# Kernel optimization log

Hardware: AMD Instinct MI355X
Metric: run time of the kernel (lower is better)

## Reference

```python
import jax, jax.numpy as jnp
import numpy as np

IN_FEATURES = 3072
OUT_FEATURES = 4096
PADDED = 4096  # 2**ceil(log2(in_features))
PADDING = PADDED - IN_FEATURES
MIN_RANGE = -384.0
MAX_RANGE = 384.0
Q_LEVELS = 255.0  # 8-bit affine quantization


def fwht(x):
    """Unnormalized fast Walsh-Hadamard transform along the last axis.
    H @ H = n * I, matching the /padded_dim rescale in forward."""
    n = x.shape[-1]
    m = int(round(np.log2(n)))
    lead = x.shape[:-1]
    x = x.reshape((-1,) + (2,) * m)
    for ax in range(1, m + 1):  # m <= 12 fixed butterfly stages
        a = jnp.take(x, 0, axis=ax)
        b = jnp.take(x, 1, axis=ax)
        x = jnp.stack([a + b, a - b], axis=ax)
    return x.reshape(lead + (n,))


def quant_dequant(x):
    """QuantizedMatrix: clip to [MIN_RANGE, MAX_RANGE], 8-bit affine
    quantize, then dequantize (reference computes the dequantized values)."""
    scale = (MAX_RANGE - MIN_RANGE) / Q_LEVELS
    q = jnp.clip(jnp.round((jnp.clip(x, MIN_RANGE, MAX_RANGE) - MIN_RANGE) / scale), 0.0, Q_LEVELS)
    return q * scale + MIN_RANGE


def setup_inputs() -> dict:
    key = jax.random.key(0)
    k1, k2, k3 = jax.random.split(key, 3)
    x = jax.random.normal(k1, (2, 4096, IN_FEATURES), dtype=jnp.float32)
    weight = jax.random.normal(k2, (OUT_FEATURES, IN_FEATURES), dtype=jnp.float32)
    bias = jax.random.normal(k3, (OUT_FEATURES,), dtype=jnp.float32)
    return {"x": x, "weight": weight, "bias": bias}


def reference(x, weight, bias):
    # pad feature dim to power of two, Hadamard-rotate activations and weights
    xh = fwht(jnp.pad(x, ((0, 0), (0, 0), (0, PADDING))))          # [B,S,P]
    wh = fwht(jnp.pad(weight, ((0, 0), (0, PADDING))))              # [O,P]
    qx = quant_dequant(xh)
    qw = quant_dequant(wh)
    # qx @ qw / padded_dim + bias  (qw contracted over the padded dim)
    return jnp.einsum('bsp,op->bso', qx, qw) / PADDED + bias
```

## Files before the change

### kernel.cpp

```cpp
#include <hip/hip_runtime.h>

typedef int v4i __attribute__((ext_vector_type(4)));
typedef int v16i __attribute__((ext_vector_type(16)));

#define IN_F   3072
#define PAD    4096
#define M_ROWS 8192
#define N_OUT  4096

#define BM 128
#define BN 256
#define BK 64

__device__ __forceinline__ void async_copy16(const void* g, void* l) {
    __builtin_amdgcn_global_load_lds(
        (__attribute__((address_space(1))) const void*)(uintptr_t)g,
        (__attribute__((address_space(3))) void*)(uint32_t)(uintptr_t)l,
        16, 0, 0);
}

__device__ __forceinline__ void fwht16(float v[16]) {
#pragma unroll
    for (int s = 1; s < 16; s <<= 1) {
#pragma unroll
        for (int i = 0; i < 16; i++) {
            if ((i & s) == 0) {
                float a = v[i], b = v[i ^ s];
                v[i]     = a + b;
                v[i ^ s] = a - b;
            }
        }
    }
}

__global__ __launch_bounds__(256) void fwht_quant_kernel(
    const float* __restrict__ in, signed char* __restrict__ qout,
    int* __restrict__ rowsum, int nrows)
{
    __shared__ float lds[4096];
    __shared__ int ssum;
    const int t = threadIdx.x;
    const int r = blockIdx.x;
    if (r >= nrows) return;
    const float* row = in + (size_t)r * IN_F;

    float v[16];
#pragma unroll
    for (int j = 0; j < 16; j++)
        v[j] = (j < 12) ? row[j * 256 + t] : 0.0f;

    fwht16(v);

    const int th = t >> 4, tl = t & 15;

    #pragma unroll
    for (int j = 0; j < 16; j++)
        lds[256 * j + 16 * (th ^ j) + (tl ^ th)] = v[j];
    __syncthreads();
#pragma unroll
    for (int j = 0; j < 16; j++)
        v[j] = lds[256 * th + 16 * (j ^ th) + (tl ^ j)];

    fwht16(v);

    if (t == 0) ssum = 0;
    __syncthreads();

#pragma unroll
    for (int j = 0; j < 16; j++)
        lds[256 * th + 16 * (j ^ th) + (tl ^ j)] = v[j];
    __syncthreads();
#pragma unroll
    for (int j = 0; j < 16; j++)
        v[j] = lds[256 * th + 16 * (tl ^ th) + (j ^ tl)];

    fwht16(v);

    const float INV = 0.33203125f;
    int sum = 0;
    int pk[4];
#pragma unroll
    for (int c = 0; c < 4; c++) {
        int word = 0;
#pragma unroll
        for (int b = 0; b < 4; b++) {
            float x = v[c * 4 + b];
            x = fminf(fmaxf(x, -384.0f), 384.0f);
            float qf = rintf((x + 384.0f) * INV);
            int qi = (int)qf;
            qi = qi < 0 ? 0 : (qi > 255 ? 255 : qi);
            int a = qi - 128;
            sum += a;
            word |= (a & 255) << (8 * b);
        }
        pk[c] = word;
    }

#pragma unroll
    for (int off = 32; off > 0; off >>= 1) sum += __shfl_down(sum, off, 64);
    if ((t & 63) == 0) atomicAdd(&ssum, sum);

    ((int4*)(qout + (size_t)r * PAD))[t] = make_int4(pk[0], pk[1], pk[2], pk[3]);

    __syncthreads();
    if (t == 0) rowsum[r] = ssum;
}

__global__ __launch_bounds__(256, 2) void gemm_i8_kernel(
    const signed char* __restrict__ A, const signed char* __restrict__ B,
    const int* __restrict__ SA, const int* __restrict__ SB,
    const float* __restrict__ bias, float* __restrict__ out,
    float kA, float kS, float kC)
{
    __shared__ __align__(16) signed char As[BM * BK];
    __shared__ __align__(16) signed char Bs[BN * BK];

    const int tid  = threadIdx.x;
    const int lane = tid & 63;
    const int wid  = tid >> 6;
    const int wr   = wid >> 1, wc = wid & 1;
    const int bm   = blockIdx.y * BM;
    const int bn   = blockIdx.x * BN;
    const int l5   = lane >> 5;
    const int lm   = lane & 31;

    v16i acc[2][4];
#pragma unroll
    for (int i = 0; i < 2; i++)
#pragma unroll
        for (int j = 0; j < 4; j++)
#pragma unroll
            for (int e = 0; e < 16; e++)
                acc[i][j][e] = 0;

    for (int bk = 0; bk < PAD; bk += BK) {
#pragma unroll
        for (int i = 0; i < 2; i++) {
            int c = wid * 128 + i * 64 + lane;
            int rr = c >> 2, p = c & 3;
            int q = (p - rr) & 3;
            async_copy16(A + (size_t)(bm + rr) * PAD + bk + q * 16,
                         As + (wid * 128 + i * 64) * 16);
        }
#pragma unroll
        for (int i = 0; i < 4; i++) {
            int c = wid * 256 + i * 64 + lane;
            int rr = c >> 2, p = c & 3;
            int q = (p - rr) & 3;
            async_copy16(B + (size_t)(bn + rr) * PAD + bk + q * 16,
                         Bs + (wid * 256 + i * 64) * 16);
        }
        __syncthreads();

#pragma unroll
        for (int ks = 0; ks < 2; ks++) {
            const int qbase = ks * 2 + l5;
            v4i a[2], b[4];
#pragma unroll
            for (int mt = 0; mt < 2; mt++) {
                int rr = wr * 64 + mt * 32 + lm;
                int p = (qbase + rr) & 3;
                a[mt] = *(const v4i*)(As + rr * 64 + p * 16);
            }
#pragma unroll
            for (int nt = 0; nt < 4; nt++) {
                int rr = wc * 128 + nt * 32 + lm;
                int p = (qbase + rr) & 3;
                b[nt] = *(const v4i*)(Bs + rr * 64 + p * 16);
            }
#pragma unroll
            for (int mt = 0; mt < 2; mt++)
#pragma unroll
                for (int nt = 0; nt < 4; nt++)
                    acc[mt][nt] = __builtin_amdgcn_mfma_i32_32x32x32_i8(
                        a[mt], b[nt], acc[mt][nt], 0, 0, 0);
        }
        __syncthreads();
    }

#pragma unroll
    for (int nt = 0; nt < 4; nt++) {
        int n = bn + wc * 128 + nt * 32 + lm;
        float ct = (float)SB[n] * kS + kC + bias[n];
#pragma unroll
        for (int mt = 0; mt < 2; mt++) {
#pragma unroll
            for (int e = 0; e < 16; e++) {
                int m = bm + wr * 64 + mt * 32 + l5 * 4 + (e & 3) + 8 * (e >> 2);
                out[(size_t)m * N_OUT + n] =
                    (float)acc[mt][nt][e] * kA + (float)SA[m] * kS + ct;
            }
        }
    }
}

extern "C" void kernel_launch(void* const* d_in, const int* in_sizes, int n_in,
                              void* d_out, int out_size, void* d_ws, size_t ws_size,
                              hipStream_t stream) {
    const float* x    = (const float*)d_in[0];
    const float* w    = (const float*)d_in[1];
    const float* bias = (const float*)d_in[2];
    float* out = (float*)d_out;

    signed char* qa = (signed char*)d_ws;
    signed char* qb = qa + (size_t)M_ROWS * PAD;
    int* SA = (int*)(qb + (size_t)N_OUT * PAD);
    int* SB = SA + M_ROWS;

    fwht_quant_kernel<<<M_ROWS, 256, 0, stream>>>(x, qa, SA, M_ROWS);
    fwht_quant_kernel<<<N_OUT,  256, 0, stream>>>(w, qb, SB, N_OUT);

    double s = 768.0 / 255.0;
    double c = 384.0 / 255.0;
    float kA = (float)(s * s / PAD);
    float kS = (float)(s * c / PAD);
    float kC = (float)(c * c);

    dim3 grid(N_OUT / BN, M_ROWS / BM);
    gemm_i8_kernel<<<grid, 256, 0, stream>>>(qa, qb, SA, SB, bias, out, kA, kS, kC);
}
```

Measured before the change: 402.5 us.

## Store quantized operands in GEMM tile-blocked layout for contiguous async loads

The FWHT/quantize kernel now writes int8 outputs in a tile-major layout, with rows grouped into BM/BN blocks and 16-byte chunks ordered by K chunk and then row. The GEMM kernel can then stream each K tile as one contiguous block and read LDS fragments without XOR swizzle arithmetic. The aim is fully coalesced global loads and less address math. The cost is scattered 16-byte stores in the quantize kernel, and the LDS reads now use a plain row stride, which may cause bank conflicts.

```diff
diff --git a/kernel.cpp b/kernel.cpp
--- a/kernel.cpp
+++ b/kernel.cpp
@@ -35,13 +35,12 @@
 
 __global__ __launch_bounds__(256) void fwht_quant_kernel(
     const float* __restrict__ in, signed char* __restrict__ qout,
-    int* __restrict__ rowsum, int nrows)
+    int* __restrict__ rowsum, int rsh, int rows)
 {
     __shared__ float lds[4096];
     __shared__ int ssum;
     const int t = threadIdx.x;
     const int r = blockIdx.x;
-    if (r >= nrows) return;
     const float* row = in + (size_t)r * IN_F;
 
     float v[16];
@@ -53,7 +52,7 @@
 
     const int th = t >> 4, tl = t & 15;
 
-    #pragma unroll
+#pragma unroll
     for (int j = 0; j < 16; j++)
         lds[256 * j + 16 * (th ^ j) + (tl ^ th)] = v[j];
     __syncthreads();
@@ -100,7 +99,8 @@
     for (int off = 32; off > 0; off >>= 1) sum += __shfl_down(sum, off, 64);
     if ((t & 63) == 0) atomicAdd(&ssum, sum);
 
-    ((int4*)(qout + (size_t)r * PAD))[t] = make_int4(pk[0], pk[1], pk[2], pk[3]);
+    size_t o16 = ((size_t)(r >> rsh) * 256 + t) * rows + (r & (rows - 1));
+    *(int4*)(qout + o16 * 16) = make_int4(pk[0], pk[1], pk[2], pk[3]);
 
     __syncthreads();
     if (t == 0) rowsum[r] = ssum;
@@ -124,6 +124,9 @@
     const int l5   = lane >> 5;
     const int lm   = lane & 31;
 
+    const signed char* aSrc = A + (size_t)blockIdx.y * 64 * (BM * BK);
+    const signed char* bSrc = B + (size_t)blockIdx.x * 64 * (BN * BK);
+
     v16i acc[2][4];
 #pragma unroll
     for (int i = 0; i < 2; i++)
@@ -133,41 +136,31 @@
             for (int e = 0; e < 16; e++)
                 acc[i][j][e] = 0;
 
-    for (int bk = 0; bk < PAD; bk += BK) {
+    for (int tk = 0; tk < 64; tk++) {
 #pragma unroll
         for (int i = 0; i < 2; i++) {
-            int c = wid * 128 + i * 64 + lane;
-            int rr = c >> 2, p = c & 3;
-            int q = (p - rr) & 3;
-            async_copy16(A + (size_t)(bm + rr) * PAD + bk + q * 16,
-                         As + (wid * 128 + i * 64) * 16);
+            int c16 = wid * 128 + i * 64 + lane;
+            async_copy16(aSrc + c16 * 16, As + (wid * 128 + i * 64) * 16);
         }
 #pragma unroll
         for (int i = 0; i < 4; i++) {
-            int c = wid * 256 + i * 64 + lane;
-            int rr = c >> 2, p = c & 3;
-            int q = (p - rr) & 3;
-            async_copy16(B + (size_t)(bn + rr) * PAD + bk + q * 16,
-                         Bs + (wid * 256 + i * 64) * 16);
-        }
+            int c16 = wid * 256 + i * 64 + lane;
+            async_copy16(bSrc + c16 * 16, Bs + (wid * 256 + i * 64) * 16);
+        }
+        aSrc += BM * BK;
+        bSrc += BN * BK;
         __syncthreads();
 
 #pragma unroll
         for (int ks = 0; ks < 2; ks++) {
-            const int qbase = ks * 2 + l5;
+            const int qb = ks * 2 + l5;
             v4i a[2], b[4];
 #pragma unroll
-            for (int mt = 0; mt < 2; mt++) {
-                int rr = wr * 64 + mt * 32 + lm;
-                int p = (qbase + rr) & 3;
-                a[mt] = *(const v4i*)(As + rr * 64 + p * 16);
-            }
-#pragma unroll
-            for (int nt = 0; nt < 4; nt++) {
-                int rr = wc * 128 + nt * 32 + lm;
-                int p = (qbase + rr) & 3;
-                b[nt] = *(const v4i*)(Bs + rr * 64 + p * 16);
-            }
+            for (int mt = 0; mt < 2; mt++)
+                a[mt] = *(const v4i*)(As + (qb * 128 + wr * 64 + mt * 32 + lm) * 16);
+#pragma unroll
+            for (int nt = 0; nt < 4; nt++)
+                b[nt] = *(const v4i*)(Bs + (qb * 256 + wc * 128 + nt * 32 + lm) * 16);
 #pragma unroll
             for (int mt = 0; mt < 2; mt++)
 #pragma unroll
@@ -207,8 +200,8 @@
     int* SA = (int*)(qb + (size_t)N_OUT * PAD);
     int* SB = SA + M_ROWS;
 
-    fwht_quant_kernel<<<M_ROWS, 256, 0, stream>>>(x, qa, SA, M_ROWS);
-    fwht_quant_kernel<<<N_OUT,  256, 0, stream>>>(w, qb, SB, N_OUT);
+    fwht_quant_kernel<<<M_ROWS, 256, 0, stream>>>(x, qa, SA, 7, BM);
+    fwht_quant_kernel<<<N_OUT,  256, 0, stream>>>(w, qb, SB, 8, BN);
 
     double s = 768.0 / 255.0;
     double c = 384.0 / 255.0;
```

Measured after the change: 411.8 us. 1.02x slower.
